# Kernel optimization log

Hardware: AMD Instinct MI355X
Metric: run time of the kernel (lower is better)

## Reference

```python
import jax, jax.numpy as jnp
import numpy as np
from jax import lax

D_MODEL = 1024
D_STATE = 16
D_CONV = 4
D_INNER = 2048  # expand * d_model
DT_RANK = 64    # ceil(d_model / 16)
BATCH = 2
SEQ = 2048


def setup_inputs() -> dict:
    key = jax.random.key(0)
    ks = jax.random.split(key, 8)
    s = 0.02
    x = jax.random.normal(ks[0], (BATCH, SEQ, D_MODEL), jnp.float32)
    in_proj_w = jax.random.normal(ks[1], (2 * D_INNER, D_MODEL), jnp.float32) * s
    conv_w = jax.random.normal(ks[2], (D_INNER, 1, D_CONV), jnp.float32) * s  # [out, in/groups, k]
    conv_b = jax.random.normal(ks[3], (D_INNER,), jnp.float32) * s
    x_proj_w = jax.random.normal(ks[4], (DT_RANK + 2 * D_STATE, D_INNER), jnp.float32) * s
    dt_proj_w = jax.random.normal(ks[5], (D_INNER, DT_RANK), jnp.float32) * s
    dt_proj_b = jax.random.normal(ks[6], (D_INNER,), jnp.float32) * s
    A_log = jnp.log(jnp.tile(jnp.arange(1, D_STATE + 1, dtype=jnp.float32), (D_INNER, 1)))
    D = jnp.ones((D_INNER,), jnp.float32)
    out_proj_w = jax.random.normal(ks[7], (D_MODEL, D_INNER), jnp.float32) * s
    return dict(x=x, in_proj_w=in_proj_w, conv_w=conv_w, conv_b=conv_b,
                x_proj_w=x_proj_w, dt_proj_w=dt_proj_w, dt_proj_b=dt_proj_b,
                A_log=A_log, D=D, out_proj_w=out_proj_w)


def _causal_depthwise_conv(x_bcl, conv_w, conv_b):
    # x_bcl: [B, d_inner, L]; conv_w: [d_inner, 1, k]; left-pad k-1 -> causal, output length L
    y = lax.conv_general_dilated(
        x_bcl, conv_w,
        window_strides=(1,), padding=[(D_CONV - 1, 0)],
        feature_group_count=D_INNER,
        dimension_numbers=('NCH', 'OIH', 'NCH'))
    return y + conv_b[None, :, None]


def _ssm(xc, x_proj_w, dt_proj_w, dt_proj_b, A_log, D):
    # xc: [B, L, d_inner]
    A = -jnp.exp(A_log)                                   # [d, N]
    x_dbl = jnp.einsum('bld,rd->blr', xc, x_proj_w)       # [B, L, dt_rank + 2N]
    dt_low = x_dbl[..., :DT_RANK]
    Bm = x_dbl[..., DT_RANK:DT_RANK + D_STATE]            # [B, L, N]
    Cm = x_dbl[..., DT_RANK + D_STATE:]                   # [B, L, N]
    dt = jax.nn.softplus(jnp.einsum('blr,dr->bld', dt_low, dt_proj_w) + dt_proj_b)  # [B, L, d]
    dA = jnp.exp(dt[..., None] * A)                       # [B, L, d, N]
    dBx = dt[..., None] * Bm[:, :, None, :] * xc[..., None]  # [B, L, d, N]

    def step(h, inp):
        dA_t, dBx_t, C_t = inp                            # [B,d,N], [B,d,N], [B,N]
        h = dA_t * h + dBx_t
        y = jnp.einsum('bdn,bn->bd', h, C_t)
        return h, y

    h0 = jnp.zeros((xc.shape[0], D_INNER, D_STATE), xc.dtype)
    _, ys = lax.scan(step, h0,
                     (dA.transpose(1, 0, 2, 3), dBx.transpose(1, 0, 2, 3), Cm.transpose(1, 0, 2)))
    y = ys.transpose(1, 0, 2)                             # [B, L, d]
    return y + xc * D


def reference(x, in_proj_w, conv_w, conv_b, x_proj_w, dt_proj_w, dt_proj_b, A_log, D, out_proj_w):
    xz = jnp.einsum('blm,om->blo', x, in_proj_w)          # [B, L, 2*d_inner]
    xs, z = jnp.split(xz, 2, axis=-1)
    xc = _causal_depthwise_conv(xs.transpose(0, 2, 1), conv_w, conv_b).transpose(0, 2, 1)
    xc = jax.nn.silu(xc)
    y = _ssm(xc, x_proj_w, dt_proj_w, dt_proj_b, A_log, D)
    out = y * jax.nn.silu(z)
    return jnp.einsum('bld,md->blm', out, out_proj_w)
```

## Files before the change

### kernel.cpp

```cpp
#include <hip/hip_runtime.h>

#define SEQ    2048
#define DIN    2048
#define DMODEL 1024
#define NROWS  4096
#define NCH    64
#define CHL    32

typedef __attribute__((ext_vector_type(8))) _Float16 half8v;
typedef __attribute__((ext_vector_type(8))) unsigned short ushort8v;
typedef __attribute__((ext_vector_type(4))) float f32x4;

__device__ __forceinline__ float sigf(float x) { return 1.0f / (1.0f + __expf(-x)); }
__device__ __forceinline__ float softplusf(float v) {
    return fmaxf(v, 0.f) + __logf(1.f + __expf(-fabsf(v)));
}

__device__ __forceinline__ void gload16(const void* g, const void* l) {
    __builtin_amdgcn_global_load_lds((const __attribute__((address_space(1))) void*)g,
                                     (__attribute__((address_space(3))) void*)l, 16, 0, 0);
}

__device__ __forceinline__ unsigned short f2h(float x) {
    _Float16 h = (_Float16)x;
    unsigned short u;
    __builtin_memcpy(&u, &h, 2);
    return u;
}
__device__ __forceinline__ float h2f(unsigned short u) {
    _Float16 h;
    __builtin_memcpy(&h, &u, 2);
    return (float)h;
}

__global__ __launch_bounds__(256) void cvt_in_k(
    const float* __restrict__ x, const float* __restrict__ wi, const float* __restrict__ wx,
    const float* __restrict__ wd, const float* __restrict__ wo,
    unsigned short* __restrict__ xh, unsigned short* __restrict__ wih,
    unsigned short* __restrict__ wxh, unsigned short* __restrict__ wdh,
    unsigned short* __restrict__ woh)
{
    int i = blockIdx.x * 256 + threadIdx.x;
    if (i < 1048576) {
        float4 v = ((const float4*)x)[i];
        ushort4 h; h.x = f2h(v.x); h.y = f2h(v.y); h.z = f2h(v.z); h.w = f2h(v.w);
        ((ushort4*)xh)[i] = h;
    } else if (i < 2097152) {
        i -= 1048576;
        float4 v = ((const float4*)wi)[i];
        ushort4 h; h.x = f2h(v.x); h.y = f2h(v.y); h.z = f2h(v.z); h.w = f2h(v.w);
        ((ushort4*)wih)[i] = h;
    } else if (i < 2162688) {
        i -= 2097152;
        int row = i >> 9, q = i & 511;
        ushort4 h;
        if (row < 96) {
            float4 v = ((const float4*)wx)[(size_t)row * 512 + q];
            h.x = f2h(v.x); h.y = f2h(v.y); h.z = f2h(v.z); h.w = f2h(v.w);
        } else h = make_ushort4(0, 0, 0, 0);
        ((ushort4*)wxh)[(size_t)row * 512 + q] = h;
    } else if (i < 2195456) {
        i -= 2162688;
        float4 v = ((const float4*)wd)[i];
        ushort4 h; h.x = f2h(v.x); h.y = f2h(v.y); h.z = f2h(v.z); h.w = f2h(v.w);
        ((ushort4*)wdh)[i] = h;
    } else {
        i -= 2195456;
        float4 v = ((const float4*)wo)[i];
        ushort4 h; h.x = f2h(v.x); h.y = f2h(v.y); h.z = f2h(v.z); h.w = f2h(v.w);
        ((ushort4*)woh)[i] = h;
    }
}

__global__ __launch_bounds__(512, 2) void gemm256_h(
    const unsigned short* __restrict__ A, const unsigned short* __restrict__ W,
    unsigned short* __restrict__ C, int K, int N, int mtiles, int lda, int ldw)
{
    __shared__ uint4 ldsu4[8192];
    char* lds = (char*)ldsu4;
    const int tid = threadIdx.x;
    const int w = tid >> 6, lane = tid & 63;

    const int nwg = gridDim.x;
    const int cpx = nwg >> 3;
    const int bid = blockIdx.x;
    const int swz = (bid & 7) * cpx + (bid >> 3);
    const int ntiles = nwg / mtiles;
    const int per = 8 * ntiles;
    const int gid = swz / per;
    const int rem = swz - gid * per;
    const int m0 = (gid * 8 + (rem & 7)) * 256;
    const int n0 = (rem >> 3) * 256;

    const int wr = w >> 2, wc = w & 3;
    const int lm = lane & 15, lk = lane >> 4;

    f32x4 acc[8][4];
#pragma unroll
    for (int i = 0; i < 8; ++i)
#pragma unroll
        for (int j = 0; j < 4; ++j) { acc[i][j][0]=0.f; acc[i][j][1]=0.f; acc[i][j][2]=0.f; acc[i][j][3]=0.f; }

    const int rsub = w * 8 + (lane >> 3);
    const int xr8  = ((lane & 7) ^ (lane >> 3)) << 3;
    const unsigned short* gA = A + (size_t)(m0 + rsub) * lda + xr8;
    const unsigned short* gW = W + (size_t)(n0 + rsub) * ldw + xr8;
    const int sdst = w * 1024;

    auto stageA = [&](int bb, int hi, int kt) {
        char* d = lds + bb * 65536 + hi * 16384 + sdst;
        const unsigned short* s = gA + (size_t)hi * 128 * lda + kt;
        gload16(s, d);
        gload16(s + (size_t)64 * lda, d + 8192);
    };
    auto stageB = [&](int bb, int hi, int kt) {
        char* d = lds + bb * 65536 + 32768 + hi * 16384 + sdst;
        const unsigned short* s = gW + (size_t)hi * 128 * ldw + kt;
        gload16(s, d);
        gload16(s + (size_t)64 * ldw, d + 8192);
    };

    half8v a[4][2], b[2][2][2];
    auto loadA = [&](int bb, int mh) {
#pragma unroll
        for (int mb = 0; mb < 4; ++mb)
#pragma unroll
            for (int kk = 0; kk < 2; ++kk) {
                int ar = wr * 128 + (mh * 4 + mb) * 16 + lm;
                a[mb][kk] = *(const half8v*)(lds + bb * 65536 + ar * 128 + (((kk * 4 + lk) ^ (lm & 7)) << 4));
            }
    };
    auto loadB = [&](int bb, int nh) {
#pragma unroll
        for (int nb = 0; nb < 2; ++nb)
#pragma unroll
            for (int kk = 0; kk < 2; ++kk) {
                int br = wc * 64 + (nh * 2 + nb) * 16 + lm;
                b[nh][nb][kk] = *(const half8v*)(lds + bb * 65536 + 32768 + br * 128 + (((kk * 4 + lk) ^ (lm & 7)) << 4));
            }
    };
    auto mm = [&](int mh, int nh) {
        __builtin_amdgcn_s_setprio(1);
#pragma unroll
        for (int mb = 0; mb < 4; ++mb)
#pragma unroll
            for (int nb = 0; nb < 2; ++nb)
#pragma unroll
                for (int kk = 0; kk < 2; ++kk)
                    acc[mh * 4 + mb][nh * 2 + nb] = __builtin_amdgcn_mfma_f32_16x16x32_f16(
                        a[mb][kk], b[nh][nb][kk], acc[mh * 4 + mb][nh * 2 + nb], 0, 0, 0);
        __builtin_amdgcn_s_setprio(0);
    };
#define BAR()  __builtin_amdgcn_s_barrier()

    stageA(0, 0, 0); stageA(0, 1, 0); stageB(0, 0, 0); stageB(0, 1, 0);
    asm volatile("s_waitcnt vmcnt(0)" ::: "memory");
    BAR();

    const int NT = K >> 6;
    for (int t = 0; t < NT - 1; ++t) {
        const int cur = t & 1, nxt = cur ^ 1;
        const int kt = (t + 1) << 6;
        stageA(nxt, 0, kt);
        asm volatile("s_waitcnt vmcnt(2)" ::: "memory");
        BAR();
        loadA(cur, 0); loadB(cur, 0);
        stageB(nxt, 0, kt);
        mm(0, 0);
        loadB(cur, 1);
        stageB(nxt, 1, kt);
        mm(0, 1);
        loadA(cur, 1);
        stageA(nxt, 1, kt);
        mm(1, 1);
        mm(1, 0);
        BAR();
    }
    {
        const int cur = (NT - 1) & 1;
        asm volatile("s_waitcnt vmcnt(0)" ::: "memory");
        BAR();
        loadA(cur, 0); loadB(cur, 0); mm(0, 0);
        loadB(cur, 1); mm(0, 1);
        loadA(cur, 1); mm(1, 1); mm(1, 0);
    }
#undef BAR

#pragma unroll
    for (int mb = 0; mb < 8; ++mb)
#pragma unroll
        for (int nb = 0; nb < 4; ++nb)
#pragma unroll
            for (int r = 0; r < 4; ++r)
                C[(size_t)(m0 + wr * 128 + mb * 16 + lk * 4 + r) * N + (n0 + wc * 64 + nb * 16 + lm)]
                    = f2h(acc[mb][nb][r]);
}

#define A_OFF 0
#define W_OFF 16384

__global__ __launch_bounds__(256) void gemm_mfma_h(
    const unsigned short* __restrict__ A, const unsigned short* __restrict__ W,
    unsigned short* __restrict__ C, int K, int ldc, int nmax, int mtiles,
    int sA1, int sA2, int ldw, const float* __restrict__ bias, int kspl, int cstride)
{
    __shared__ uint4 ldsu4[2048];
    char* lds = (char*)ldsu4;
    const int tid  = threadIdx.x;
    const int w    = tid >> 6, lane = tid & 63;

    const int nwg = gridDim.x;
    const int cpx = nwg >> 3;
    const int bid = blockIdx.x;
    const int swz = (bid & 7) * cpx + (bid >> 3);
    const int nbp = nwg / kspl;
    const int ks  = swz / nbp;
    const int tt  = swz - ks * nbp;
    const int ntiles = nbp / mtiles;
    const int per = 8 * ntiles;
    const int gid = tt / per;
    const int rem = tt - gid * per;
    const int m0 = (gid * 8 + (rem & 7)) * 128;
    const int n0 = (rem >> 3) * 128;
    const int kOff = ks * K;

    const int wr = w >> 1, wc = w & 1;

    f32x4 acc[4][4];
#pragma unroll
    for (int i = 0; i < 4; ++i)
#pragma unroll
        for (int j = 0; j < 4; ++j) { acc[i][j][0]=0.f; acc[i][j][1]=0.f; acc[i][j][2]=0.f; acc[i][j][3]=0.f; }

    const int rloc = w * 32 + (lane >> 3);
    const int xr8  = ((lane & 7) ^ (lane >> 3)) << 3;
    const int rowA = m0 + rloc;
    const unsigned short* gA = A + (size_t)(rowA >> 1) * sA2 + (size_t)(rowA & 1) * sA1 + kOff + xr8;
    const unsigned short* gW = W + (size_t)(n0 + rloc) * ldw + kOff + xr8;

    const int lm  = lane & 15;
    const int lk  = lane >> 4;
    const int lk4 = lk * 4;

    for (int kt = 0; kt < K; kt += 64) {
#pragma unroll
        for (int i = 0; i < 4; ++i) {
            const int rb = w * 32 + i * 8;
            gload16(gA + (size_t)i * 4 * sA2 + kt, lds + A_OFF + rb * 128);
            gload16(gW + (size_t)i * 8 * ldw + kt, lds + W_OFF + rb * 128);
        }
        __syncthreads();
#pragma unroll
        for (int h = 0; h < 2; ++h) {
            half8v af[4], wf[4];
            const int ch = h * 4 + lk;
#pragma unroll
            for (int t = 0; t < 4; ++t) {
                const int ar = wr * 64 + t * 16 + lm;
                const int wrw = wc * 64 + t * 16 + lm;
                af[t] = *(const half8v*)(lds + A_OFF + ar * 128 + ((ch ^ (ar & 7)) << 4));
                wf[t] = *(const half8v*)(lds + W_OFF + wrw * 128 + ((ch ^ (wrw & 7)) << 4));
            }
#pragma unroll
            for (int i = 0; i < 4; ++i)
#pragma unroll
                for (int j = 0; j < 4; ++j)
                    acc[i][j] = __builtin_amdgcn_mfma_f32_16x16x32_f16(af[i], wf[j], acc[i][j], 0, 0, 0);
        }
        __syncthreads();
    }

    unsigned short* Cp = C + (size_t)ks * cstride;
    if (bias) {
#pragma unroll
        for (int j = 0; j < 4; ++j) {
            const int n = n0 + wc * 64 + j * 16 + lm;
            const float bv = (n < nmax) ? bias[n] : 0.f;
#pragma unroll
            for (int i = 0; i < 4; ++i)
#pragma unroll
                for (int r = 0; r < 4; ++r) {
                    float v = acc[i][j][r] + bv;
                    if (n < nmax)
                        Cp[(size_t)(m0 + wr * 64 + i * 16 + lk4 + r) * ldc + n] = f2h(softplusf(v));
                }
        }
    } else {
#pragma unroll
        for (int i = 0; i < 4; ++i)
#pragma unroll
            for (int j = 0; j < 4; ++j) {
                const int n = n0 + wc * 64 + j * 16 + lm;
                if (n < nmax)
#pragma unroll
                    for (int r = 0; r < 4; ++r)
                        Cp[(size_t)(m0 + wr * 64 + i * 16 + lk4 + r) * ldc + n] = f2h(acc[i][j][r]);
            }
    }
}

__global__ __launch_bounds__(256) void xproj_reduce_k(
    const unsigned short* __restrict__ part, float* __restrict__ xdbl,
    unsigned short* __restrict__ dlh)
{
    int i = blockIdx.x * 256 + threadIdx.x;
    if (i >= NROWS * 32) return;
    int row = i >> 5, q = i & 31;
    float s0 = 0.f, s1 = 0.f, s2 = 0.f, s3 = 0.f;
#pragma unroll
    for (int ks = 0; ks < 8; ++ks) {
        ushort4 v = *(const ushort4*)(part + (size_t)ks * (NROWS * 128) + (size_t)row * 128 + q * 4);
        s0 += h2f(v.x); s1 += h2f(v.y); s2 += h2f(v.z); s3 += h2f(v.w);
    }
    if (q < 16) {
        ushort4 h; h.x = f2h(s0); h.y = f2h(s1); h.z = f2h(s2); h.w = f2h(s3);
        *(ushort4*)(dlh + (size_t)row * 64 + q * 4) = h;
    } else {
        *(float4*)(xdbl + (size_t)row * 96 + q * 4) = make_float4(s0, s1, s2, s3);
    }
}

__global__ __launch_bounds__(256) void out_reduce_k(
    const unsigned short* __restrict__ p, float* __restrict__ out)
{
    int i = blockIdx.x * 256 + threadIdx.x;
    ushort4 a = ((const ushort4*)p)[i];
    ushort4 b = ((const ushort4*)(p + 4194304))[i];
    float4 v;
    v.x = h2f(a.x) + h2f(b.x);
    v.y = h2f(a.y) + h2f(b.y);
    v.z = h2f(a.z) + h2f(b.z);
    v.w = h2f(a.w) + h2f(b.w);
    ((float4*)out)[i] = v;
}

__global__ __launch_bounds__(256) void conv_silu_k(
    const unsigned short* __restrict__ xzh, const float* __restrict__ cw,
    const float* __restrict__ cb, unsigned short* __restrict__ xch)
{
    int i = blockIdx.x * 256 + threadIdx.x;
    int d8 = (i & 255) << 3;
    int row = i >> 8;
    int l = row & (SEQ - 1);
    const unsigned short* base = xzh + (size_t)row * 4096 + d8;
    ushort8v x0 = *(const ushort8v*)base;
    ushort8v x1 = {}, x2 = {}, x3 = {};
    if (l >= 1) x1 = *(const ushort8v*)(base - 4096);
    if (l >= 2) x2 = *(const ushort8v*)(base - 8192);
    if (l >= 3) x3 = *(const ushort8v*)(base - 12288);
    ushort8v out;
#pragma unroll
    for (int j = 0; j < 8; ++j) {
        float4 wv = *(const float4*)(cw + (size_t)(d8 + j) * 4);
        float a = cb[d8 + j];
        a = fmaf(h2f(x3[j]), wv.x, a);
        a = fmaf(h2f(x2[j]), wv.y, a);
        a = fmaf(h2f(x1[j]), wv.z, a);
        a = fmaf(h2f(x0[j]), wv.w, a);
        out[j] = f2h(a * sigf(a));
    }
    *(ushort8v*)(xch + (size_t)row * DIN + d8) = out;
}

__global__ __launch_bounds__(256) void scan_pass1(
    const unsigned short* __restrict__ dth, const unsigned short* __restrict__ xch,
    const float* __restrict__ xdbl, const float* __restrict__ Alog,
    float* __restrict__ hbuf, float* __restrict__ apbuf)
{
    const int b = blockIdx.z, c = blockIdx.y;
    const int d = blockIdx.x * 256 + threadIdx.x;
    float A[16];
#pragma unroll
    for (int q = 0; q < 4; ++q) *(float4*)&A[q * 4] = *(const float4*)&Alog[(size_t)d * 16 + q * 4];
    bool seq = true;
#pragma unroll
    for (int n = 0; n < 16; ++n) {
        A[n] = -__expf(A[n]);
        seq = seq && (fabsf(A[n] + (float)(n + 1)) < 1e-5f * (float)(n + 1));
    }
    float h[16] = {};
    float sumdt = 0.f;
    const int rowbase = b * SEQ + c * CHL;
    int row = rowbase;
    float dtv = h2f(dth[(size_t)row * DIN + d]);
    float xcv = h2f(xch[(size_t)row * DIN + d]);
    if (seq) {
        for (int t = 0; t < CHL; ++t) {
            const int nrow = row + ((t + 1) < CHL ? 1 : 0);
            float dtv2 = h2f(dth[(size_t)nrow * DIN + d]);
            float xcv2 = h2f(xch[(size_t)nrow * DIN + d]);
            const float* xr = xdbl + (size_t)row * 96;
            float u = dtv * xcv;
            sumdt += dtv;
            float r = __expf(-dtv);
            float dA = r;
#pragma unroll
            for (int n = 0; n < 16; ++n) {
                h[n] = fmaf(dA, h[n], u * xr[64 + n]);
                dA *= r;
            }
            dtv = dtv2; xcv = xcv2; row = nrow;
        }
    } else {
        for (int t = 0; t < CHL; ++t) {
            const int nrow = row + ((t + 1) < CHL ? 1 : 0);
            float dtv2 = h2f(dth[(size_t)nrow * DIN + d]);
            float xcv2 = h2f(xch[(size_t)nrow * DIN + d]);
            const float* xr = xdbl + (size_t)row * 96;
            float u = dtv * xcv;
            sumdt += dtv;
#pragma unroll
            for (int n = 0; n < 16; ++n) {
                float dA = __expf(dtv * A[n]);
                h[n] = fmaf(dA, h[n], u * xr[64 + n]);
            }
            dtv = dtv2; xcv = xcv2; row = nrow;
        }
    }
    float ap[16];
    if (seq) {
        float R = __expf(-sumdt);
        float a = R;
#pragma unroll
        for (int n = 0; n < 16; ++n) { ap[n] = a; a *= R; }
    } else {
#pragma unroll
        for (int n = 0; n < 16; ++n) ap[n] = __expf(sumdt * A[n]);
    }
    size_t e = ((size_t)(b * NCH + c) << 15) + (size_t)d * 16;
#pragma unroll
    for (int q = 0; q < 4; ++q) {
        *(float4*)(hbuf + e + q * 4)  = *(float4*)&h[q * 4];
        *(float4*)(apbuf + e + q * 4) = *(float4*)&ap[q * 4];
    }
}

__global__ __launch_bounds__(256) void scan_pass2(
    float* __restrict__ hbuf, const float* __restrict__ apbuf)
{
    int idx = blockIdx.x * 256 + threadIdx.x;
    int b = idx >> 15;
    int dn = idx & 32767;
    float carry = 0.f;
    for (int c = 0; c < NCH; ++c) {
        size_t e = ((size_t)(b * NCH + c) << 15) + dn;
        float hl = hbuf[e];
        float ap = apbuf[e];
        hbuf[e] = carry;
        carry = fmaf(ap, carry, hl);
    }
}

__global__ __launch_bounds__(256) void scan_pass3(
    const unsigned short* __restrict__ dth, const unsigned short* __restrict__ xch,
    const unsigned short* __restrict__ xzh, const float* __restrict__ xdbl,
    const float* __restrict__ Alog, const float* __restrict__ Dp,
    const float* __restrict__ hbuf, unsigned short* __restrict__ oph)
{
    const int b = blockIdx.z, c = blockIdx.y;
    const int d = blockIdx.x * 256 + threadIdx.x;
    float A[16];
#pragma unroll
    for (int q = 0; q < 4; ++q) *(float4*)&A[q * 4] = *(const float4*)&Alog[(size_t)d * 16 + q * 4];
    bool seq = true;
#pragma unroll
    for (int n = 0; n < 16; ++n) {
        A[n] = -__expf(A[n]);
        seq = seq && (fabsf(A[n] + (float)(n + 1)) < 1e-5f * (float)(n + 1));
    }
    float h[16];
    size_t e = ((size_t)(b * NCH + c) << 15) + (size_t)d * 16;
#pragma unroll
    for (int q = 0; q < 4; ++q) *(float4*)&h[q * 4] = *(const float4*)(hbuf + e + q * 4);
    const float Dd = Dp[d];
    const int rowbase = b * SEQ + c * CHL;
    int row = rowbase;
    float dtv = h2f(dth[(size_t)row * DIN + d]);
    float xcv = h2f(xch[(size_t)row * DIN + d]);
    float zv  = h2f(xzh[(size_t)row * 4096 + DIN + d]);
    if (seq) {
        for (int t = 0; t < CHL; ++t) {
            const int nrow = row + ((t + 1) < CHL ? 1 : 0);
            float dtv2 = h2f(dth[(size_t)nrow * DIN + d]);
            float xcv2 = h2f(xch[(size_t)nrow * DIN + d]);
            float zv2  = h2f(xzh[(size_t)nrow * 4096 + DIN + d]);
            const float* xr = xdbl + (size_t)row * 96;
            float u = dtv * xcv;
            float r = __expf(-dtv);
            float dA = r;
            float y = 0.f;
#pragma unroll
            for (int n = 0; n < 16; ++n) {
                h[n] = fmaf(dA, h[n], u * xr[64 + n]);
                y = fmaf(h[n], xr[80 + n], y);
                dA *= r;
            }
            float val = (y + xcv * Dd) * zv * sigf(zv);
            oph[(size_t)row * DIN + d] = f2h(val);
            dtv = dtv2; xcv = xcv2; zv = zv2; row = nrow;
        }
    } else {
        for (int t = 0; t < CHL; ++t) {
            const int nrow = row + ((t + 1) < CHL ? 1 : 0);
            float dtv2 = h2f(dth[(size_t)nrow * DIN + d]);
            float xcv2 = h2f(xch[(size_t)nrow * DIN + d]);
            float zv2  = h2f(xzh[(size_t)nrow * 4096 + DIN + d]);
            const float* xr = xdbl + (size_t)row * 96;
            float u = dtv * xcv;
            float y = 0.f;
#pragma unroll
            for (int n = 0; n < 16; ++n) {
                float dA = __expf(dtv * A[n]);
                h[n] = fmaf(dA, h[n], u * xr[64 + n]);
                y = fmaf(h[n], xr[80 + n], y);
            }
            float val = (y + xcv * Dd) * zv * sigf(zv);
            oph[(size_t)row * DIN + d] = f2h(val);
            dtv = dtv2; xcv = xcv2; zv = zv2; row = nrow;
        }
    }
}

extern "C" void kernel_launch(void* const* d_in, const int* in_sizes, int n_in,
                              void* d_out, int out_size, void* d_ws, size_t ws_size,
                              hipStream_t stream)
{
    const float* x    = (const float*)d_in[0];
    const float* wi   = (const float*)d_in[1];
    const float* cw   = (const float*)d_in[2];
    const float* cb   = (const float*)d_in[3];
    const float* wx   = (const float*)d_in[4];
    const float* wd   = (const float*)d_in[5];
    const float* bd   = (const float*)d_in[6];
    const float* alog = (const float*)d_in[7];
    const float* Dp   = (const float*)d_in[8];
    const float* wo   = (const float*)d_in[9];
    float* out = (float*)d_out;

    float* wsf  = (float*)d_ws;
    float* xzr  = wsf;
    float* xcr  = wsf + 16777216;
    float* xdbl = wsf + 25165824;
    float* dtr  = wsf + 25559040;

    unsigned short* xzh = (unsigned short*)xzr;
    float* scr = xzr + 8388608;
    unsigned short* oph = (unsigned short*)scr;
    float* hbuf         = scr + 4194304;

    unsigned short* xh  = (unsigned short*)xcr;
    unsigned short* xch = (unsigned short*)xcr;
    float* apbuf        = xcr + 4194304;

    unsigned short* wih    = (unsigned short*)dtr;
    unsigned short* dth    = (unsigned short*)dtr;
    unsigned short* oparth = (unsigned short*)dtr;
    unsigned short* wxh    = (unsigned short*)(dtr + 4194304);
    unsigned short* xparth = (unsigned short*)(dtr + 4325376);
    unsigned short* woh    = (unsigned short*)(dtr + 6422528);
    unsigned short* wdh    = (unsigned short*)(dtr + 7471104);
    unsigned short* dlh    = (unsigned short*)(dtr + 7536640);

    cvt_in_k<<<10624, 256, 0, stream>>>(x, wi, wx, wd, wo, xh, wih, wxh, wdh, woh);
    gemm256_h<<<256, 512, 0, stream>>>(xh, wih, xzh, 1024, 4096, 16, 1024, 1024);
    conv_silu_k<<<4096, 256, 0, stream>>>(xzh, cw, cb, xch);
    gemm_mfma_h<<<256, 256, 0, stream>>>(xch, wxh, xparth, 256, 128, 128, 32, 2048, 4096, 2048,
                                         nullptr, 8, NROWS * 128);
    xproj_reduce_k<<<512, 256, 0, stream>>>(xparth, xdbl, dlh);
    gemm_mfma_h<<<512, 256, 0, stream>>>(dlh, wdh, dth, 64, 2048, 2048, 32, 64, 128, 64,
                                         bd, 1, 0);
    scan_pass1<<<dim3(8, NCH, 2), 256, 0, stream>>>(dth, xch, xdbl, alog, hbuf, apbuf);
    scan_pass2<<<256, 256, 0, stream>>>(hbuf, apbuf);
    scan_pass3<<<dim3(8, NCH, 2), 256, 0, stream>>>(dth, xch, xzh, xdbl, alog, Dp, hbuf, oph);
    gemm_mfma_h<<<512, 256, 0, stream>>>(oph, woh, oparth, 1024, 1024, 1024, 32, 2048, 4096, 2048,
                                         nullptr, 2, 4194304);
    out_reduce_k<<<4096, 256, 0, stream>>>(oparth, out);
}
```

Baseline: 193.7 us.

## Shrink in-proj GEMM tile to 256x128 with single-buffered LDS and higher occupancy

Replaces the double-buffered, hand-interleaved 256x256 in-projection GEMM with a simpler 256x128 tile that uses a single LDS buffer and two __syncthreads per K step. The grid doubles to 512 workgroups and launch bounds request 4 waves-per-EU occupancy, relying on more resident workgroups to hide latency instead of explicit prefetch. The cost is lost load/compute overlap inside each block and lower arithmetic intensity per tile, since each A tile is now loaded twice across N.

```diff
diff --git a/kernel.cpp b/kernel.cpp
--- a/kernel.cpp
+++ b/kernel.cpp
@@ -72,11 +72,11 @@
     }
 }
 
-__global__ __launch_bounds__(512, 2) void gemm256_h(
+__global__ __launch_bounds__(512, 4) void gemm_inproj(
     const unsigned short* __restrict__ A, const unsigned short* __restrict__ W,
     unsigned short* __restrict__ C, int K, int N, int mtiles, int lda, int ldw)
 {
-    __shared__ uint4 ldsu4[8192];
+    __shared__ uint4 ldsu4[3072];
     char* lds = (char*)ldsu4;
     const int tid = threadIdx.x;
     const int w = tid >> 6, lane = tid & 63;
@@ -90,16 +90,16 @@
     const int gid = swz / per;
     const int rem = swz - gid * per;
     const int m0 = (gid * 8 + (rem & 7)) * 256;
-    const int n0 = (rem >> 3) * 256;
+    const int n0 = (rem >> 3) * 128;
 
     const int wr = w >> 2, wc = w & 3;
     const int lm = lane & 15, lk = lane >> 4;
 
-    f32x4 acc[8][4];
+    f32x4 acc[8][2];
 #pragma unroll
     for (int i = 0; i < 8; ++i)
 #pragma unroll
-        for (int j = 0; j < 4; ++j) { acc[i][j][0]=0.f; acc[i][j][1]=0.f; acc[i][j][2]=0.f; acc[i][j][3]=0.f; }
+        for (int j = 0; j < 2; ++j) { acc[i][j][0]=0.f; acc[i][j][1]=0.f; acc[i][j][2]=0.f; acc[i][j][3]=0.f; }
 
     const int rsub = w * 8 + (lane >> 3);
     const int xr8  = ((lane & 7) ^ (lane >> 3)) << 3;
@@ -107,92 +107,43 @@
     const unsigned short* gW = W + (size_t)(n0 + rsub) * ldw + xr8;
     const int sdst = w * 1024;
 
-    auto stageA = [&](int bb, int hi, int kt) {
-        char* d = lds + bb * 65536 + hi * 16384 + sdst;
-        const unsigned short* s = gA + (size_t)hi * 128 * lda + kt;
-        gload16(s, d);
-        gload16(s + (size_t)64 * lda, d + 8192);
-    };
-    auto stageB = [&](int bb, int hi, int kt) {
-        char* d = lds + bb * 65536 + 32768 + hi * 16384 + sdst;
-        const unsigned short* s = gW + (size_t)hi * 128 * ldw + kt;
-        gload16(s, d);
-        gload16(s + (size_t)64 * ldw, d + 8192);
-    };
-
-    half8v a[4][2], b[2][2][2];
-    auto loadA = [&](int bb, int mh) {
-#pragma unroll
-        for (int mb = 0; mb < 4; ++mb)
-#pragma unroll
-            for (int kk = 0; kk < 2; ++kk) {
-                int ar = wr * 128 + (mh * 4 + mb) * 16 + lm;
-                a[mb][kk] = *(const half8v*)(lds + bb * 65536 + ar * 128 + (((kk * 4 + lk) ^ (lm & 7)) << 4));
-            }
-    };
-    auto loadB = [&](int bb, int nh) {
+    for (int kt = 0; kt < K; kt += 64) {
+#pragma unroll
+        for (int i = 0; i < 4; ++i)
+            gload16(gA + (size_t)i * 64 * lda + kt, lds + i * 8192 + sdst);
+#pragma unroll
+        for (int i = 0; i < 2; ++i)
+            gload16(gW + (size_t)i * 64 * ldw + kt, lds + 32768 + i * 8192 + sdst);
+        __syncthreads();
+#pragma unroll
+        for (int kk = 0; kk < 2; ++kk) {
+            half8v b[2];
+#pragma unroll
+            for (int nb = 0; nb < 2; ++nb) {
+                const int br = wc * 32 + nb * 16 + lm;
+                b[nb] = *(const half8v*)(lds + 32768 + br * 128 + (((kk * 4 + lk) ^ (br & 7)) << 4));
+            }
+            __builtin_amdgcn_s_setprio(1);
+#pragma unroll
+            for (int mb = 0; mb < 8; ++mb) {
+                const int ar = wr * 128 + mb * 16 + lm;
+                half8v a = *(const half8v*)(lds + ar * 128 + (((kk * 4 + lk) ^ (ar & 7)) << 4));
+#pragma unroll
+                for (int nb = 0; nb < 2; ++nb)
+                    acc[mb][nb] = __builtin_amdgcn_mfma_f32_16x16x32_f16(a, b[nb], acc[mb][nb], 0, 0, 0);
+            }
+            __builtin_amdgcn_s_setprio(0);
+        }
+        __syncthreads();
+    }
+
+#pragma unroll
+    for (int mb = 0; mb < 8; ++mb)
 #pragma unroll
         for (int nb = 0; nb < 2; ++nb)
 #pragma unroll
-            for (int kk = 0; kk < 2; ++kk) {
-                int br = wc * 64 + (nh * 2 + nb) * 16 + lm;
-                b[nh][nb][kk] = *(const half8v*)(lds + bb * 65536 + 32768 + br * 128 + (((kk * 4 + lk) ^ (lm & 7)) << 4));
-            }
-    };
-    auto mm = [&](int mh, int nh) {
-        __builtin_amdgcn_s_setprio(1);
-#pragma unroll
-        for (int mb = 0; mb < 4; ++mb)
-#pragma unroll
-            for (int nb = 0; nb < 2; ++nb)
-#pragma unroll
-                for (int kk = 0; kk < 2; ++kk)
-                    acc[mh * 4 + mb][nh * 2 + nb] = __builtin_amdgcn_mfma_f32_16x16x32_f16(
-                        a[mb][kk], b[nh][nb][kk], acc[mh * 4 + mb][nh * 2 + nb], 0, 0, 0);
-        __builtin_amdgcn_s_setprio(0);
-    };
-#define BAR()  __builtin_amdgcn_s_barrier()
-
-    stageA(0, 0, 0); stageA(0, 1, 0); stageB(0, 0, 0); stageB(0, 1, 0);
-    asm volatile("s_waitcnt vmcnt(0)" ::: "memory");
-    BAR();
-
-    const int NT = K >> 6;
-    for (int t = 0; t < NT - 1; ++t) {
-        const int cur = t & 1, nxt = cur ^ 1;
-        const int kt = (t + 1) << 6;
-        stageA(nxt, 0, kt);
-        asm volatile("s_waitcnt vmcnt(2)" ::: "memory");
-        BAR();
-        loadA(cur, 0); loadB(cur, 0);
-        stageB(nxt, 0, kt);
-        mm(0, 0);
-        loadB(cur, 1);
-        stageB(nxt, 1, kt);
-        mm(0, 1);
-        loadA(cur, 1);
-        stageA(nxt, 1, kt);
-        mm(1, 1);
-        mm(1, 0);
-        BAR();
-    }
-    {
-        const int cur = (NT - 1) & 1;
-        asm volatile("s_waitcnt vmcnt(0)" ::: "memory");
-        BAR();
-        loadA(cur, 0); loadB(cur, 0); mm(0, 0);
-        loadB(cur, 1); mm(0, 1);
-        loadA(cur, 1); mm(1, 1); mm(1, 0);
-    }
-#undef BAR
-
-#pragma unroll
-    for (int mb = 0; mb < 8; ++mb)
-#pragma unroll
-        for (int nb = 0; nb < 4; ++nb)
-#pragma unroll
             for (int r = 0; r < 4; ++r)
-                C[(size_t)(m0 + wr * 128 + mb * 16 + lk * 4 + r) * N + (n0 + wc * 64 + nb * 16 + lm)]
+                C[(size_t)(m0 + wr * 128 + mb * 16 + lk * 4 + r) * N + (n0 + wc * 32 + nb * 16 + lm)]
                     = f2h(acc[mb][nb][r]);
 }
 
@@ -562,7 +513,7 @@
     unsigned short* dlh    = (unsigned short*)(dtr + 7536640);
 
     cvt_in_k<<<10624, 256, 0, stream>>>(x, wi, wx, wd, wo, xh, wih, wxh, wdh, woh);
-    gemm256_h<<<256, 512, 0, stream>>>(xh, wih, xzh, 1024, 4096, 16, 1024, 1024);
+    gemm_inproj<<<512, 512, 0, stream>>>(xh, wih, xzh, 1024, 4096, 16, 1024, 1024);
     conv_silu_k<<<4096, 256, 0, stream>>>(xzh, cw, cb, xch);
     gemm_mfma_h<<<256, 256, 0, stream>>>(xch, wxh, xparth, 256, 128, 128, 32, 2048, 4096, 2048,
                                          nullptr, 8, NROWS * 128);
```

New measurement: 196.1 us. About the same (+1.2%).
